# Optimization experiments

Hardware: AMD Instinct MI355X
Metric: run time of the kernel (lower is better)

The kernel has to match this reference:

```python
import jax, jax.numpy as jnp
import numpy as np

N, E, F, H, C, G = 50000, 800000, 20, 4, 64, 64
D = H * C           # 256 = hidden_dim * heads
OUT = 256
L = 6               # 3 res blocks x depth 2 GATv2 layers
NEG_SLOPE = 0.2     # PyG GATv2Conv default negative_slope


def setup_inputs() -> dict:
    key = jax.random.key(0)
    ks = jax.random.split(key, 16)
    def nrm(k, shape, fan_in):
        return jax.random.normal(k, shape, jnp.float32) * (1.0 / np.sqrt(fan_in))
    return {
        "x": jax.random.normal(ks[0], (N, F), jnp.float32),
        "pos": jax.random.normal(ks[1], (N, 3), jnp.float32) * 10.0,
        "edge_index": jax.random.randint(ks[2], (2, E), 0, N),
        "batch": jnp.sort(jax.random.randint(ks[3], (N,), 0, G)),
        # edge_MLP1 = MLP([1, 32, 1])
        "mlp_w1": nrm(ks[4], (1, 32), 1),
        "mlp_b1": jnp.zeros((32,), jnp.float32),
        "mlp_w2": nrm(ks[5], (32, 1), 32),
        "mlp_b2": jnp.zeros((1,), jnp.float32),
        "w_in": nrm(ks[6], (F, D), F),
        "b_in": jnp.zeros((D,), jnp.float32),
        # 6 stacked GATv2Conv layers (all in=D, heads=H, out-per-head=C)
        "gat_wl": nrm(ks[7], (L, D, D), D),
        "gat_bl": jnp.zeros((L, D), jnp.float32),
        "gat_wr": nrm(ks[8], (L, D, D), D),
        "gat_br": jnp.zeros((L, D), jnp.float32),
        "gat_we": nrm(ks[9], (L, 1, D), 1),      # lin_edge, edge_dim=1, no bias
        "gat_att": nrm(ks[10], (L, H, C), C),
        "gat_bias": jnp.zeros((L, D), jnp.float32),
        # 3 AttentionalAggregation modules: gate_nn=Linear(D,1), nn=Linear(D,D)
        "gate_w": nrm(ks[11], (3, D, 1), D),
        "gate_b": jnp.zeros((3, 1), jnp.float32),
        "nn_w": nrm(ks[12], (3, D, D), D),
        "nn_b": jnp.zeros((3, D), jnp.float32),
        "out_w1": nrm(ks[13], (3 * D, OUT), 3 * D),
        "out_b1": jnp.zeros((OUT,), jnp.float32),
        "out_w2": nrm(ks[14], (OUT, OUT), OUT),
        "out_b2": jnp.zeros((OUT,), jnp.float32),
    }


def _segment_softmax(logits, seg, num_segments):
    m = jax.ops.segment_max(logits, seg, num_segments=num_segments)
    e = jnp.exp(logits - m[seg])
    s = jax.ops.segment_sum(e, seg, num_segments=num_segments)
    return e / (s[seg] + 1e-16)


def _gatv2(h, src, dst, ew, wl, bl, wr, br, we, att, bias):
    # h: [N, D]; ew: [E, 1] edge features
    n = h.shape[0]
    xl = (h @ wl + bl).reshape(n, H, C)           # source-side transform (x_j)
    xr = (h @ wr + br).reshape(n, H, C)           # target-side transform (x_i)
    ee = (ew @ we).reshape(-1, H, C)              # edge transform (no bias)
    xj = xl[src]                                  # [E, H, C]
    g = jax.nn.leaky_relu(xj + xr[dst] + ee, NEG_SLOPE)
    alpha = jnp.einsum('ehc,hc->eh', g, att)      # [E, H]
    alpha = _segment_softmax(alpha, dst, n)       # softmax over incoming edges
    out = jax.ops.segment_sum(xj * alpha[:, :, None], dst, num_segments=n)
    return out.reshape(n, D) + bias


def _agg(h, batch, gw, gb, nw, nb):
    gate = _segment_softmax((h @ gw + gb)[:, 0], batch, G)     # [N]
    v = h @ nw + nb
    return jax.ops.segment_sum(gate[:, None] * v, batch, num_segments=G)


def _forward(x, pos, mlp_w1, mlp_b1, mlp_w2, mlp_b2, w_in, b_in,
             gat_wl, gat_bl, gat_wr, gat_br, gat_we, gat_att, gat_bias,
             gate_w, gate_b, nn_w, nn_b, out_w1, out_b1, out_w2, out_b2,
             edge_index, batch):
    src, dst = edge_index[0], edge_index[1]
    d = jnp.linalg.norm(pos[src] - pos[dst], axis=1)[:, None]          # [E,1]
    ew = jax.nn.relu(jax.nn.relu(d @ mlp_w1 + mlp_b1) @ mlp_w2 + mlp_b2)  # [E,1]
    h = x @ w_in + b_in                                                # [N,D]
    outs = []
    for blk in range(3):
        for j in range(2):
            i = blk * 2 + j
            h = h + _gatv2(h, src, dst, ew, gat_wl[i], gat_bl[i], gat_wr[i],
                           gat_br[i], gat_we[i], gat_att[i], gat_bias[i])
            h = jax.nn.relu(h)   # Dropout -> identity (eval mode)
        outs.append(_agg(h, batch, gate_w[blk], gate_b[blk], nn_w[blk], nn_b[blk]))
    z = jnp.concatenate(outs, axis=1)                                  # [G, 3D]
    enc = jax.nn.relu(z @ out_w1 + out_b1) @ out_w2 + out_b2
    return h, enc


def reference(x, pos, edge_index, batch, mlp_w1, mlp_b1, mlp_w2, mlp_b2,
              w_in, b_in, gat_wl, gat_bl, gat_wr, gat_br, gat_we, gat_att,
              gat_bias, gate_w, gate_b, nn_w, nn_b, out_w1, out_b1,
              out_w2, out_b2):
    return _forward(x, pos, mlp_w1, mlp_b1, mlp_w2, mlp_b2, w_in, b_in,
                    gat_wl, gat_bl, gat_wr, gat_br, gat_we, gat_att, gat_bias,
                    gate_w, gate_b, nn_w, nn_b, out_w1, out_b1, out_w2, out_b2,
                    edge_index, batch)
```

## Files before the change

### kernel.cpp

```cpp
#include <hip/hip_runtime.h>
#include <math.h>

constexpr int F_IN = 20;
constexpr int DDIM = 256;

typedef __attribute__((ext_vector_type(8))) short bf16x8;
typedef __attribute__((ext_vector_type(4))) float f32x4;

__device__ __forceinline__ float lrelu(float x){ return x > 0.f ? x : 0.2f*x; }

__device__ __forceinline__ float b2f(unsigned short u){
  union { unsigned int i; float f; } x; x.i = ((unsigned int)u) << 16; return x.f;
}
__device__ __forceinline__ unsigned short f2b(float f){
  union { float f; unsigned int i; } x; x.f = f;
  unsigned int r = x.i + 0x7fffu + ((x.i >> 16) & 1u);
  return (unsigned short)(r >> 16);
}

__global__ __launch_bounds__(256) void edge_prep_k(
    const int* __restrict__ ei, const float* __restrict__ pos,
    const float* __restrict__ mw1, const float* __restrict__ mb1,
    const float* __restrict__ mw2, const float* __restrict__ mb2,
    float* __restrict__ ew, int* __restrict__ cnt, int E)
{
  int t = blockIdx.x*256 + threadIdx.x;
  if (t >= E) return;
  int s = ei[t], d = ei[E + t];
  float dx = pos[s*3+0]-pos[d*3+0];
  float dy = pos[s*3+1]-pos[d*3+1];
  float dz = pos[s*3+2]-pos[d*3+2];
  float dist = sqrtf(dx*dx+dy*dy+dz*dz);
  float o = mb2[0];
  #pragma unroll
  for (int j=0;j<32;j++){
    float hj = fmaxf(dist*mw1[j]+mb1[j], 0.f);
    o += hj*mw2[j];
  }
  o = fmaxf(o, 0.f);
  ew[t] = o;
  atomicAdd(&cnt[d], 1);
}

__global__ __launch_bounds__(512) void scan1_k(const int* __restrict__ cnt, int* __restrict__ offs,
                                               int* __restrict__ bsum, int n)
{
  __shared__ int t[512];
  int tid = threadIdx.x;
  int i = blockIdx.x*512 + tid;
  int v = (i < n) ? cnt[i] : 0;
  t[tid] = v;
  __syncthreads();
  for (int s = 1; s < 512; s <<= 1) {
    int y = (tid >= s) ? t[tid - s] : 0;
    __syncthreads();
    if (tid >= s) t[tid] += y;
    __syncthreads();
  }
  if (i < n) offs[i] = t[tid] - v;
  if (tid == 511) bsum[blockIdx.x] = t[511];
}

__global__ __launch_bounds__(512) void scan2_k(const int* __restrict__ bsum, int* __restrict__ bpre, int nb)
{
  __shared__ int t[512];
  int tid = threadIdx.x;
  int v = (tid < nb) ? bsum[tid] : 0;
  t[tid] = v;
  __syncthreads();
  for (int s = 1; s < 512; s <<= 1) {
    int y = (tid >= s) ? t[tid - s] : 0;
    __syncthreads();
    if (tid >= s) t[tid] += y;
    __syncthreads();
  }
  bpre[tid] = t[tid] - v;
}

__global__ __launch_bounds__(512) void scan3_k(int* __restrict__ offs, const int* __restrict__ bpre, int n, int e)
{
  int i = blockIdx.x*512 + threadIdx.x;
  if (i < n) offs[i] += bpre[blockIdx.x];
  if (i == 0) offs[n] = e;
}

__global__ __launch_bounds__(256) void scatter_k(const int* __restrict__ ei, const float* __restrict__ ew,
    int* __restrict__ cur, int* __restrict__ ssrc, float* __restrict__ sew, int E)
{
  int t = blockIdx.x*256 + threadIdx.x;
  if (t >= E) return;
  int d = ei[E+t];
  int p = atomicAdd(&cur[d], 1);
  ssrc[p] = ei[t];
  sew[p] = ew[t];
}

__global__ void gseg_k(const int* __restrict__ batch, int* __restrict__ goff, int n){
  int g = threadIdx.x;
  if (g > 64) return;
  int lo = 0, hi = n;
  while (lo < hi){ int mid = (lo + hi) >> 1; if (batch[mid] < g) lo = mid + 1; else hi = mid; }
  goff[g] = lo;
}

__global__ __launch_bounds__(256) void wt_k(const float* __restrict__ gwl, const float* __restrict__ gwr,
                                            unsigned short* __restrict__ Wt)
{
  __shared__ float t[64][65];
  int ct = blockIdx.x;
  int kt = blockIdx.y;
  int layer = blockIdx.z;
  int tid = threadIdx.x;
  int cbase = ct*64, k0 = kt*64;
  const float* src = (cbase < 256) ? (gwl + (size_t)layer*65536) : (gwr + (size_t)layer*65536);
  int csrc0 = (cbase < 256) ? cbase : cbase - 256;
  #pragma unroll
  for (int j = 0; j < 16; ++j){
    int idx = j*256 + tid;
    int kl = idx >> 6, cl = idx & 63;
    t[cl][kl] = src[(size_t)(k0 + kl)*256 + csrc0 + cl];
  }
  __syncthreads();
  #pragma unroll
  for (int j = 0; j < 16; ++j){
    int idx = j*256 + tid;
    int cl = idx >> 6, kl = idx & 63;
    Wt[(size_t)layer*131072 + (size_t)(cbase + cl)*256 + k0 + kl] = f2b(t[cl][kl]);
  }
}

__global__ __launch_bounds__(256) void h0_k(const float* __restrict__ x, const float* __restrict__ w,
    const float* __restrict__ b, float* __restrict__ h, unsigned short* __restrict__ hb, int n)
{
  __shared__ float xs[16][20];
  int row0 = blockIdx.x*16, tid = threadIdx.x;
  for (int idx = tid; idx < 16*20; idx += 256){
    int r = idx/20, c = idx%20;
    int rr = row0 + r;
    xs[r][c] = (rr < n) ? x[rr*20 + c] : 0.f;
  }
  __syncthreads();
  float bj = b[tid];
  float acc[16];
  #pragma unroll
  for (int r=0;r<16;r++) acc[r] = bj;
  for (int k=0;k<20;k++){
    float wv = w[k*256 + tid];
    #pragma unroll
    for (int r=0;r<16;r++) acc[r] += xs[r][k]*wv;
  }
  #pragma unroll
  for (int r=0;r<16;r++){
    int rr = row0 + r;
    if (rr < n){
      h[(size_t)rr*256 + tid] = acc[r];
      hb[(size_t)rr*256 + tid] = f2b(acc[r]);
    }
  }
}

__global__ __launch_bounds__(256) void gemm_mfma_k(
    const unsigned short* __restrict__ hb,
    const unsigned short* __restrict__ Wt,
    const float* __restrict__ bl, const float* __restrict__ br,
    unsigned short* __restrict__ out,
    int n)
{
  __shared__ short As[128*64];
  __shared__ short Bs[128*64];
  int tid = threadIdx.x;
  int lane = tid & 63, wid = tid >> 6;
  int wr = wid >> 1, wc = wid & 1;
  int row0 = blockIdx.x * 128;
  int col0 = blockIdx.y * 128;
  f32x4 acc[4][4] = {};

  for (int k0 = 0; k0 < 256; k0 += 64) {
    #pragma unroll
    for (int j = 0; j < 4; ++j) {
      int c = j*256 + tid;
      int r = c >> 3, q = c & 7;
      int rg = row0 + r; if (rg > n-1) rg = n-1;
      bf16x8 av = *(const bf16x8*)(hb + (size_t)rg*256 + k0 + q*8);
      bf16x8 bv = *(const bf16x8*)(Wt + (size_t)(col0 + r)*256 + k0 + q*8);
      int qs = (q ^ (r & 7)) * 8;
      *(bf16x8*)(As + r*64 + qs) = av;
      *(bf16x8*)(Bs + r*64 + qs) = bv;
    }
    __syncthreads();
    #pragma unroll
    for (int kk = 0; kk < 2; ++kk) {
      bf16x8 a[4], b[4];
      #pragma unroll
      for (int mi = 0; mi < 4; ++mi) {
        int r = wr*64 + mi*16 + (lane & 15);
        int q = (kk*4 + (lane >> 4)) ^ (r & 7);
        a[mi] = *(const bf16x8*)(As + r*64 + q*8);
      }
      #pragma unroll
      for (int ni = 0; ni < 4; ++ni) {
        int r = wc*64 + ni*16 + (lane & 15);
        int q = (kk*4 + (lane >> 4)) ^ (r & 7);
        b[ni] = *(const bf16x8*)(Bs + r*64 + q*8);
      }
      #pragma unroll
      for (int mi = 0; mi < 4; ++mi)
        #pragma unroll
        for (int ni = 0; ni < 4; ++ni)
          acc[mi][ni] = __builtin_amdgcn_mfma_f32_16x16x32_bf16(a[mi], b[ni], acc[mi][ni], 0, 0, 0);
    }
    __syncthreads();
  }

  const float* bias = (col0 < 256) ? bl : br;
  int cb = (col0 < 256) ? col0 : col0 - 256;
  #pragma unroll
  for (int ni = 0; ni < 4; ++ni) {
    int coff = wc*64 + ni*16 + (lane & 15);
    int col = col0 + coff;
    float bv = bias[cb + coff];
    #pragma unroll
    for (int mi = 0; mi < 4; ++mi) {
      #pragma unroll
      for (int e = 0; e < 4; ++e) {
        int row = row0 + wr*64 + mi*16 + (lane >> 4)*4 + e;
        if (row < n) out[(size_t)row*512 + col] = f2b(acc[mi][ni][e] + bv);
      }
    }
  }
}

__global__ __launch_bounds__(256) void gat_agg_k(
    const unsigned short* __restrict__ xlr,
    const int* __restrict__ offs, const int* __restrict__ ssrc, const float* __restrict__ sew,
    const float* __restrict__ we, const float* __restrict__ att, const float* __restrict__ bias,
    float* __restrict__ h, unsigned short* __restrict__ hb, float* __restrict__ hout,
    const float* __restrict__ gw, const float* __restrict__ gb, float* __restrict__ logit, int n)
{
  int wid = blockIdx.x*4 + (threadIdx.x >> 6);
  if (wid >= n) return;
  int lane = threadIdx.x & 63;
  int g = lane >> 4, l = lane & 15;
  int c0 = l*16;

  float xr[16], wef[16], atf[16];
  {
    const unsigned short* xrp = xlr + (size_t)wid*512 + 256 + c0;
    bf16x8 r0 = *(const bf16x8*)xrp;
    bf16x8 r1 = *(const bf16x8*)(xrp + 8);
    #pragma unroll
    for (int i=0;i<8;i++){ xr[i] = b2f((unsigned short)r0[i]); xr[8+i] = b2f((unsigned short)r1[i]); }
    #pragma unroll
    for (int q=0;q<4;q++){
      float4 wv = *(const float4*)(we + c0 + q*4);
      float4 av = *(const float4*)(att + c0 + q*4);
      wef[q*4+0]=wv.x; wef[q*4+1]=wv.y; wef[q*4+2]=wv.z; wef[q*4+3]=wv.w;
      atf[q*4+0]=av.x; atf[q*4+1]=av.y; atf[q*4+2]=av.z; atf[q*4+3]=av.w;
    }
  }

  float m = -1e30f, s = 0.f;
  float a[16];
  #pragma unroll
  for (int i=0;i<16;i++) a[i] = 0.f;

  int k = offs[wid] + g, kend = offs[wid+1];
  int src; float ewv = 0.f;
  bf16x8 xa = {0,0,0,0,0,0,0,0};
  bf16x8 xb = {0,0,0,0,0,0,0,0};
  if (k < kend){
    src = ssrc[k]; ewv = sew[k];
    const unsigned short* xp = xlr + (size_t)src*512 + c0;
    xa = *(const bf16x8*)xp; xb = *(const bf16x8*)(xp + 8);
  }
  while (__any(k < kend)) {
    bool act = (k < kend);
    bf16x8 ca = xa, cb = xb; float ce = ewv;
    k += 4;
    if (k < kend){
      src = ssrc[k]; ewv = sew[k];
      const unsigned short* xp = xlr + (size_t)src*512 + c0;
      xa = *(const bf16x8*)xp; xb = *(const bf16x8*)(xp + 8);
    }
    float xjf[16];
    #pragma unroll
    for (int i=0;i<8;i++){ xjf[i] = b2f((unsigned short)ca[i]); xjf[8+i] = b2f((unsigned short)cb[i]); }
    float p = 0.f;
    #pragma unroll
    for (int i=0;i<16;i++){
      float t = fmaf(ce, wef[i], xjf[i] + xr[i]);
      t = fmaxf(t, 0.2f*t);
      p = fmaf(t, atf[i], p);
    }
    p += __shfl_xor(p, 1);
    p += __shfl_xor(p, 2);
    if (!act) p = -1e30f;
    if (__any(p > m + 8.f)) {
      float mn = fmaxf(m, p);
      float corr = __expf(m - mn);
      float wv = act ? __expf(p - mn) : 0.f;
      s = s*corr + wv;
      #pragma unroll
      for (int i=0;i<16;i++) a[i] = fmaf(a[i], corr, wv*xjf[i]);
      m = mn;
    } else {
      float wv = act ? __expf(p - m) : 0.f;
      s += wv;
      #pragma unroll
      for (int i=0;i<16;i++) a[i] = fmaf(wv, xjf[i], a[i]);
    }
  }

  #pragma unroll
  for (int d = 16; d <= 32; d <<= 1) {
    float mo = __shfl_xor(m, d);
    float so = __shfl_xor(s, d);
    float mn = fmaxf(m, mo);
    float cs = __expf(m - mn), co = __expf(mo - mn);
    s = s*cs + so*co;
    #pragma unroll
    for (int i=0;i<16;i++){
      float ao = __shfl_xor(a[i], d);
      a[i] = fmaf(a[i], cs, ao*co);
    }
    m = mn;
  }

  float inv = 1.f/(s + 1e-16f);
  float4 av;
  if (g == 0)      av = make_float4(a[0], a[1], a[2], a[3]);
  else if (g == 1) av = make_float4(a[4], a[5], a[6], a[7]);
  else if (g == 2) av = make_float4(a[8], a[9], a[10], a[11]);
  else             av = make_float4(a[12], a[13], a[14], a[15]);
  int cw = l*16 + g*4;
  size_t base = (size_t)wid*256 + cw;
  float4 hv = *(const float4*)(h + base);
  float4 b4 = *(const float4*)(bias + cw);
  float4 o;
  o.x = fmaxf(hv.x + av.x*inv + b4.x, 0.f);
  o.y = fmaxf(hv.y + av.y*inv + b4.y, 0.f);
  o.z = fmaxf(hv.z + av.z*inv + b4.z, 0.f);
  o.w = fmaxf(hv.w + av.w*inv + b4.w, 0.f);
  *(float4*)(h + base) = o;
  ushort4 ob;
  ob.x = f2b(o.x); ob.y = f2b(o.y); ob.z = f2b(o.z); ob.w = f2b(o.w);
  *(ushort4*)(hb + base) = ob;
  if (hout) *(float4*)(hout + base) = o;

  if (gw) {
    float4 gv = *(const float4*)(gw + cw);
    float p = o.x*gv.x + o.y*gv.y + o.z*gv.z + o.w*gv.w;
    p += __shfl_xor(p, 1);
    p += __shfl_xor(p, 2);
    p += __shfl_xor(p, 4);
    p += __shfl_xor(p, 8);
    p += __shfl_xor(p, 16);
    p += __shfl_xor(p, 32);
    if (lane == 0) logit[wid] = p + gb[0];
  }
}

__global__ __launch_bounds__(1024) void pool_k(const unsigned short* __restrict__ hb,
    const float* __restrict__ logit, const int* __restrict__ goff, float* __restrict__ hbar)
{
  __shared__ float red[1024];
  __shared__ float mS, sS;
  int g = blockIdx.x, tid = threadIdx.x;
  int b0 = goff[g], b1 = goff[g+1];
  float lm = -INFINITY;
  for (int i = b0 + tid; i < b1; i += 1024) lm = fmaxf(lm, logit[i]);
  red[tid] = lm;
  __syncthreads();
  for (int s = 512; s > 0; s >>= 1){
    if (tid < s) red[tid] = fmaxf(red[tid], red[tid+s]);
    __syncthreads();
  }
  if (tid == 0) mS = red[0];
  __syncthreads();
  float m = mS;
  float sw = 0.f;
  for (int i = b0 + tid; i < b1; i += 1024) sw += __expf(logit[i] - m);
  __syncthreads();
  red[tid] = sw;
  __syncthreads();
  for (int s = 512; s > 0; s >>= 1){
    if (tid < s) red[tid] += red[tid+s];
    __syncthreads();
  }
  if (tid == 0) sS = red[0];
  __syncthreads();
  float sden = sS;
  int ch = tid & 255, rs = tid >> 8;
  float acc = 0.f;
  for (int i = b0 + rs; i < b1; i += 4)
    acc += __expf(logit[i] - m) * b2f(hb[(size_t)i*256 + ch]);
  __syncthreads();
  red[tid] = acc;
  __syncthreads();
  if (rs == 0){
    float a = red[ch] + red[256+ch] + red[512+ch] + red[768+ch];
    hbar[g*256 + ch] = a/(sden + 1e-16f);
  }
}

template<int K, bool RELU>
__global__ __launch_bounds__(256) void rowgemm_k(const float* __restrict__ A, const float* __restrict__ W,
    const float* __restrict__ bias, float* __restrict__ out, int ostride)
{
  __shared__ float ar[K];
  int row = blockIdx.x;
  int tid = threadIdx.x;
  for (int i = tid; i < K; i += 256) ar[i] = A[(size_t)row*K + i];
  __syncthreads();
  float acc = bias[tid];
  for (int k = 0; k < K; ++k) acc += ar[k]*W[k*256 + tid];
  if (RELU) acc = fmaxf(acc, 0.f);
  out[(size_t)row*ostride + tid] = acc;
}

extern "C" void kernel_launch(void* const* d_in, const int* in_sizes, int n_in,
                              void* d_out, int out_size, void* d_ws, size_t ws_size,
                              hipStream_t stream)
{
  const float* x     = (const float*)d_in[0];
  const float* pos   = (const float*)d_in[1];
  const int*   ei    = (const int*)d_in[2];
  const int*   batch = (const int*)d_in[3];
  const float* mw1   = (const float*)d_in[4];
  const float* mb1   = (const float*)d_in[5];
  const float* mw2   = (const float*)d_in[6];
  const float* mb2   = (const float*)d_in[7];
  const float* w_in  = (const float*)d_in[8];
  const float* b_in  = (const float*)d_in[9];
  const float* gwl   = (const float*)d_in[10];
  const float* gbl   = (const float*)d_in[11];
  const float* gwr   = (const float*)d_in[12];
  const float* gbr   = (const float*)d_in[13];
  const float* gwe   = (const float*)d_in[14];
  const float* gatt  = (const float*)d_in[15];
  const float* gbias = (const float*)d_in[16];
  const float* gate_w= (const float*)d_in[17];
  const float* gate_b= (const float*)d_in[18];
  const float* nn_w  = (const float*)d_in[19];
  const float* nn_b  = (const float*)d_in[20];
  const float* ow1   = (const float*)d_in[21];
  const float* ob1   = (const float*)d_in[22];
  const float* ow2   = (const float*)d_in[23];
  const float* ob2   = (const float*)d_in[24];

  const int N = in_sizes[0] / F_IN;
  const int E = in_sizes[2] / 2;

  char* ws = (char*)d_ws;
  size_t woff = 0;
  auto alloc = [&](size_t bytes) -> void* {
    void* p = ws + woff;
    woff = (woff + bytes + 255) & ~(size_t)255;
    return p;
  };
  float* ew    = (float*)alloc((size_t)E*4);
  int*   cnt   = (int*)  alloc((size_t)N*4);
  int*   offs  = (int*)  alloc((size_t)(N+1)*4);
  int*   cur   = (int*)  alloc((size_t)N*4);
  int*   bsum  = (int*)  alloc(512*4);
  int*   bpre  = (int*)  alloc(512*4);
  int*   ssrc  = (int*)  alloc((size_t)E*4);
  float* sew   = (float*)alloc((size_t)E*4);
  float* h     = (float*)alloc((size_t)N*DDIM*4);
  unsigned short* hb  = (unsigned short*)alloc((size_t)N*DDIM*2);
  unsigned short* xlr = (unsigned short*)alloc((size_t)N*512*2);
  unsigned short* Wt  = (unsigned short*)alloc((size_t)6*512*256*2);
  float* logit = (float*)alloc((size_t)N*4);
  int*   goff  = (int*)  alloc(68*4);
  float* hbar  = (float*)alloc(64*DDIM*4);
  float* zcat  = (float*)alloc(64*768*4);
  float* t1    = (float*)alloc(64*DDIM*4);
  (void)ws_size; (void)n_in; (void)out_size;

  hipMemsetAsync(cnt, 0, (size_t)N*4, stream);

  int eb = (E + 255)/256;
  edge_prep_k<<<eb, 256, 0, stream>>>(ei, pos, mw1, mb1, mw2, mb2, ew, cnt, E);
  int nb = (N + 511)/512;
  scan1_k<<<nb, 512, 0, stream>>>(cnt, offs, bsum, N);
  scan2_k<<<1, 512, 0, stream>>>(bsum, bpre, nb);
  scan3_k<<<nb, 512, 0, stream>>>(offs, bpre, N, E);
  hipMemcpyAsync(cur, offs, (size_t)N*4, hipMemcpyDeviceToDevice, stream);
  scatter_k<<<eb, 256, 0, stream>>>(ei, ew, cur, ssrc, sew, E);

  gseg_k<<<1, 128, 0, stream>>>(batch, goff, N);
  wt_k<<<dim3(8,4,6), 256, 0, stream>>>(gwl, gwr, Wt);

  h0_k<<<(N + 15)/16, 256, 0, stream>>>(x, w_in, b_in, h, hb, N);

  int gx = (N + 127)/128;
  int wavegrid = (N + 3)/4;
  for (int i = 0; i < 6; ++i) {
    gemm_mfma_k<<<dim3(gx, 4), 256, 0, stream>>>(hb, Wt + (size_t)i*131072,
        gbl + i*256, gbr + i*256, xlr, N);
    float* hout = (i == 5) ? (float*)d_out : (float*)nullptr;
    int blk = i >> 1;
    const float* gwp = (i & 1) ? (gate_w + blk*256) : (const float*)nullptr;
    const float* gbp = (i & 1) ? (gate_b + blk) : (const float*)nullptr;
    gat_agg_k<<<wavegrid, 256, 0, stream>>>(xlr, offs, ssrc, sew,
        gwe + i*256, gatt + i*256, gbias + i*256, h, hb, hout, gwp, gbp, logit, N);
    if (i & 1) {
      pool_k<<<64, 1024, 0, stream>>>(hb, logit, goff, hbar);
      rowgemm_k<256,false><<<64, 256, 0, stream>>>(hbar, nn_w + (size_t)blk*65536,
          nn_b + blk*256, zcat + blk*256, 768);
    }
  }
  rowgemm_k<768,true><<<64, 256, 0, stream>>>(zcat, ow1, ob1, t1, 256);
  rowgemm_k<256,false><<<64, 256, 0, stream>>>(t1, ow2, ob2, (float*)d_out + (size_t)N*DDIM, 256);
}
```

Before: 1.305 ms.

## Use direct global-to-LDS loads in GEMM and packed FP32 math in GAT aggregation

The GEMM tile staging now uses global_load_lds to copy 16-byte chunks straight into shared memory with an XOR swizzle on the source column, instead of going through registers. The GAT aggregation kernel switches to packed v_pk_fma/add/mul f32 operations on pairs, unpacks bf16 words two at a time, and replaces the 4-lane shuffle reduction with DPP moves. It also uses 32-bit offsets for the gather addresses. These target VGPR traffic and ALU issue count in the two hottest kernels. The LDS-direct load has to line up with the swizzled read pattern, so any layout mismatch would corrupt the GEMM.

Measured after the change: 1.358 ms. 1.04x slower.

```diff
diff --git a/kernel.cpp b/kernel.cpp
--- a/kernel.cpp
+++ b/kernel.cpp
@@ -6,8 +6,8 @@
 
 typedef __attribute__((ext_vector_type(8))) short bf16x8;
 typedef __attribute__((ext_vector_type(4))) float f32x4;
-
-__device__ __forceinline__ float lrelu(float x){ return x > 0.f ? x : 0.2f*x; }
+typedef __attribute__((ext_vector_type(2))) float f32x2;
+typedef __attribute__((ext_vector_type(4))) unsigned int u32x4;
 
 __device__ __forceinline__ float b2f(unsigned short u){
   union { unsigned int i; float f; } x; x.i = ((unsigned int)u) << 16; return x.f;
@@ -16,6 +16,29 @@
   union { float f; unsigned int i; } x; x.f = f;
   unsigned int r = x.i + 0x7fffu + ((x.i >> 16) & 1u);
   return (unsigned short)(r >> 16);
+}
+
+__device__ __forceinline__ f32x2 pk_add(f32x2 a, f32x2 b){ f32x2 d; asm("v_pk_add_f32 %0, %1, %2" : "=v"(d) : "v"(a), "v"(b)); return d; }
+__device__ __forceinline__ f32x2 pk_mul(f32x2 a, f32x2 b){ f32x2 d; asm("v_pk_mul_f32 %0, %1, %2" : "=v"(d) : "v"(a), "v"(b)); return d; }
+__device__ __forceinline__ f32x2 pk_fma(f32x2 a, f32x2 b, f32x2 c){ f32x2 d; asm("v_pk_fma_f32 %0, %1, %2, %3" : "=v"(d) : "v"(a), "v"(b), "v"(c)); return d; }
+
+__device__ __forceinline__ f32x2 unpk(unsigned int w){
+  union { unsigned int u; float f; } lo, hi;
+  lo.u = w << 16; hi.u = w & 0xFFFF0000u;
+  f32x2 r; r.x = lo.f; r.y = hi.f; return r;
+}
+
+__device__ __forceinline__ float dpp_sum4(float p){
+  int q1 = __builtin_amdgcn_mov_dpp(__float_as_int(p), 0xB1, 0xF, 0xF, true);
+  p += __int_as_float(q1);
+  int q2 = __builtin_amdgcn_mov_dpp(__float_as_int(p), 0x4E, 0xF, 0xF, true);
+  return p + __int_as_float(q2);
+}
+
+__device__ __forceinline__ void gload_lds16(const unsigned short* g, unsigned short* l){
+  __builtin_amdgcn_global_load_lds(
+      (const __attribute__((address_space(1))) void*)g,
+      (__attribute__((address_space(3))) void*)l, 16, 0, 0);
 }
 
 __global__ __launch_bounds__(256) void edge_prep_k(
@@ -175,17 +198,17 @@
   int col0 = blockIdx.y * 128;
   f32x4 acc[4][4] = {};
 
+  int rl = lane >> 3;
+  int csw = ((lane & 7) ^ rl) * 8;
+
   for (int k0 = 0; k0 < 256; k0 += 64) {
     #pragma unroll
-    for (int j = 0; j < 4; ++j) {
-      int c = j*256 + tid;
-      int r = c >> 3, q = c & 7;
-      int rg = row0 + r; if (rg > n-1) rg = n-1;
-      bf16x8 av = *(const bf16x8*)(hb + (size_t)rg*256 + k0 + q*8);
-      bf16x8 bv = *(const bf16x8*)(Wt + (size_t)(col0 + r)*256 + k0 + q*8);
-      int qs = (q ^ (r & 7)) * 8;
-      *(bf16x8*)(As + r*64 + qs) = av;
-      *(bf16x8*)(Bs + r*64 + qs) = bv;
+    for (int s = 0; s < 4; ++s) {
+      int S = wid*4 + s;
+      int ra = row0 + S*8 + rl; if (ra > n-1) ra = n-1;
+      gload_lds16(hb + (size_t)ra*256 + k0 + csw, (unsigned short*)(As + S*512));
+      int rb = col0 + S*8 + rl;
+      gload_lds16(Wt + (size_t)rb*256 + k0 + csw, (unsigned short*)(Bs + S*512));
     }
     __syncthreads();
     #pragma unroll
@@ -243,71 +266,78 @@
   int g = lane >> 4, l = lane & 15;
   int c0 = l*16;
 
-  float xr[16], wef[16], atf[16];
+  f32x2 xr2[8], we2[8], at2[8];
   {
-    const unsigned short* xrp = xlr + (size_t)wid*512 + 256 + c0;
-    bf16x8 r0 = *(const bf16x8*)xrp;
-    bf16x8 r1 = *(const bf16x8*)(xrp + 8);
-    #pragma unroll
-    for (int i=0;i<8;i++){ xr[i] = b2f((unsigned short)r0[i]); xr[8+i] = b2f((unsigned short)r1[i]); }
+    const u32x4* xrp = (const u32x4*)(xlr + (size_t)wid*512 + 256 + c0);
+    u32x4 r0 = xrp[0], r1 = xrp[1];
+    #pragma unroll
+    for (int j=0;j<4;j++){ xr2[j] = unpk(r0[j]); xr2[4+j] = unpk(r1[j]); }
     #pragma unroll
     for (int q=0;q<4;q++){
       float4 wv = *(const float4*)(we + c0 + q*4);
       float4 av = *(const float4*)(att + c0 + q*4);
-      wef[q*4+0]=wv.x; wef[q*4+1]=wv.y; wef[q*4+2]=wv.z; wef[q*4+3]=wv.w;
-      atf[q*4+0]=av.x; atf[q*4+1]=av.y; atf[q*4+2]=av.z; atf[q*4+3]=av.w;
-    }
-  }
+      we2[q*2+0].x=wv.x; we2[q*2+0].y=wv.y; we2[q*2+1].x=wv.z; we2[q*2+1].y=wv.w;
+      at2[q*2+0].x=av.x; at2[q*2+0].y=av.y; at2[q*2+1].x=av.z; at2[q*2+1].y=av.w;
+    }
+  }
+  const f32x2 k02 = {0.2f, 0.2f};
 
   float m = -1e30f, s = 0.f;
-  float a[16];
-  #pragma unroll
-  for (int i=0;i<16;i++) a[i] = 0.f;
+  f32x2 a2[8];
+  #pragma unroll
+  for (int j=0;j<8;j++){ a2[j].x = 0.f; a2[j].y = 0.f; }
 
   int k = offs[wid] + g, kend = offs[wid+1];
-  int src; float ewv = 0.f;
-  bf16x8 xa = {0,0,0,0,0,0,0,0};
-  bf16x8 xb = {0,0,0,0,0,0,0,0};
+  float ewv = 0.f;
+  u32x4 xa = {0,0,0,0};
+  u32x4 xbv = {0,0,0,0};
   if (k < kend){
-    src = ssrc[k]; ewv = sew[k];
-    const unsigned short* xp = xlr + (size_t)src*512 + c0;
-    xa = *(const bf16x8*)xp; xb = *(const bf16x8*)(xp + 8);
+    unsigned off = (unsigned)ssrc[k] << 9;
+    ewv = sew[k];
+    const u32x4* xp = (const u32x4*)(xlr + off + c0);
+    xa = xp[0]; xbv = xp[1];
   }
   while (__any(k < kend)) {
     bool act = (k < kend);
-    bf16x8 ca = xa, cb = xb; float ce = ewv;
+    u32x4 ca = xa, cb = xbv; float ce = ewv;
     k += 4;
     if (k < kend){
-      src = ssrc[k]; ewv = sew[k];
-      const unsigned short* xp = xlr + (size_t)src*512 + c0;
-      xa = *(const bf16x8*)xp; xb = *(const bf16x8*)(xp + 8);
-    }
-    float xjf[16];
-    #pragma unroll
-    for (int i=0;i<8;i++){ xjf[i] = b2f((unsigned short)ca[i]); xjf[8+i] = b2f((unsigned short)cb[i]); }
-    float p = 0.f;
-    #pragma unroll
-    for (int i=0;i<16;i++){
-      float t = fmaf(ce, wef[i], xjf[i] + xr[i]);
-      t = fmaxf(t, 0.2f*t);
-      p = fmaf(t, atf[i], p);
-    }
-    p += __shfl_xor(p, 1);
-    p += __shfl_xor(p, 2);
+      unsigned off = (unsigned)ssrc[k] << 9;
+      ewv = sew[k];
+      const u32x4* xp = (const u32x4*)(xlr + off + c0);
+      xa = xp[0]; xbv = xp[1];
+    }
+    f32x2 xj2[8];
+    #pragma unroll
+    for (int j=0;j<4;j++){ xj2[j] = unpk(ca[j]); xj2[4+j] = unpk(cb[j]); }
+    f32x2 ce2; ce2.x = ce; ce2.y = ce;
+    f32x2 p2; p2.x = 0.f; p2.y = 0.f;
+    #pragma unroll
+    for (int j=0;j<8;j++){
+      f32x2 t = pk_fma(ce2, we2[j], pk_add(xj2[j], xr2[j]));
+      f32x2 u = pk_mul(t, k02);
+      t.x = fmaxf(t.x, u.x); t.y = fmaxf(t.y, u.y);
+      p2 = pk_fma(t, at2[j], p2);
+    }
+    float p = p2.x + p2.y;
+    p = dpp_sum4(p);
     if (!act) p = -1e30f;
     if (__any(p > m + 8.f)) {
       float mn = fmaxf(m, p);
       float corr = __expf(m - mn);
       float wv = act ? __expf(p - mn) : 0.f;
       s = s*corr + wv;
+      f32x2 c2; c2.x = corr; c2.y = corr;
+      f32x2 w2; w2.x = wv;   w2.y = wv;
       #pragma unroll
-      for (int i=0;i<16;i++) a[i] = fmaf(a[i], corr, wv*xjf[i]);
+      for (int j=0;j<8;j++) a2[j] = pk_fma(a2[j], c2, pk_mul(w2, xj2[j]));
       m = mn;
     } else {
       float wv = act ? __expf(p - m) : 0.f;
       s += wv;
+      f32x2 w2; w2.x = wv; w2.y = wv;
       #pragma unroll
-      for (int i=0;i<16;i++) a[i] = fmaf(wv, xjf[i], a[i]);
+      for (int j=0;j<8;j++) a2[j] = pk_fma(w2, xj2[j], a2[j]);
     }
   }
 
@@ -318,29 +348,33 @@
     float mn = fmaxf(m, mo);
     float cs = __expf(m - mn), co = __expf(mo - mn);
     s = s*cs + so*co;
-    #pragma unroll
-    for (int i=0;i<16;i++){
-      float ao = __shfl_xor(a[i], d);
-      a[i] = fmaf(a[i], cs, ao*co);
+    f32x2 cs2; cs2.x = cs; cs2.y = cs;
+    f32x2 co2; co2.x = co; co2.y = co;
+    #pragma unroll
+    for (int j=0;j<8;j++){
+      f32x2 ao;
+      ao.x = __shfl_xor(a2[j].x, d);
+      ao.y = __shfl_xor(a2[j].y, d);
+      a2[j] = pk_add(pk_mul(a2[j], cs2), pk_mul(ao, co2));
     }
     m = mn;
   }
 
   float inv = 1.f/(s + 1e-16f);
-  float4 av;
-  if (g == 0)      av = make_float4(a[0], a[1], a[2], a[3]);
-  else if (g == 1) av = make_float4(a[4], a[5], a[6], a[7]);
-  else if (g == 2) av = make_float4(a[8], a[9], a[10], a[11]);
-  else             av = make_float4(a[12], a[13], a[14], a[15]);
+  f32x2 alo, ahi;
+  if (g == 0)      { alo = a2[0]; ahi = a2[1]; }
+  else if (g == 1) { alo = a2[2]; ahi = a2[3]; }
+  else if (g == 2) { alo = a2[4]; ahi = a2[5]; }
+  else             { alo = a2[6]; ahi = a2[7]; }
   int cw = l*16 + g*4;
   size_t base = (size_t)wid*256 + cw;
   float4 hv = *(const float4*)(h + base);
   float4 b4 = *(const float4*)(bias + cw);
   float4 o;
-  o.x = fmaxf(hv.x + av.x*inv + b4.x, 0.f);
-  o.y = fmaxf(hv.y + av.y*inv + b4.y, 0.f);
-  o.z = fmaxf(hv.z + av.z*inv + b4.z, 0.f);
-  o.w = fmaxf(hv.w + av.w*inv + b4.w, 0.f);
+  o.x = fmaxf(hv.x + alo.x*inv + b4.x, 0.f);
+  o.y = fmaxf(hv.y + alo.y*inv + b4.y, 0.f);
+  o.z = fmaxf(hv.z + ahi.x*inv + b4.z, 0.f);
+  o.w = fmaxf(hv.w + ahi.y*inv + b4.w, 0.f);
   *(float4*)(h + base) = o;
   ushort4 ob;
   ob.x = f2b(o.x); ob.y = f2b(o.y); ob.z = f2b(o.z); ob.w = f2b(o.w);
```
